# Kernel optimization log

Hardware: AMD Instinct MI355X
Metric: run time of the kernel (lower is better)

## Reference

```python
import jax, jax.numpy as jnp
import numpy as np
import math

NFREQ = 257
NFILTERS = 64
IN_DIM = 64
HIDDEN = 128
SR = 16000
B = 2
T = 1000


def _mel_bounds():
    # Exact replica of FreqCompression.__init__ bound computation (htk mel scale).
    all_freqs = np.linspace(0.0, SR // 2, NFREQ)
    m_max = 2595.0 * math.log10(1.0 + (SR / 2.0) / 700.0)
    m_pts = np.linspace(0.0, m_max, NFILTERS + 2)
    f_pts = 700.0 * (10.0 ** (m_pts / 2595.0) - 1.0)
    bounds = [0]
    for i in range(1, NFILTERS + 1):
        bounds.append(int(np.argmax(all_freqs > f_pts[i])))
    bounds.append(NFREQ)
    return bounds


def setup_inputs() -> dict:
    key = jax.random.key(0)
    k1, k2 = jax.random.split(key)
    bounds = _mel_bounds()
    widths = np.array([bounds[f + 2] - bounds[f] for f in range(NFILTERS)])
    jmax = int(widths.max())
    starts = np.array(bounds[:NFILTERS])
    # per-band freq-bin gather indices, clamped padding
    idx = np.clip(starts[:, None] + np.arange(jmax)[None, :], 0, NFREQ - 1)
    mask = (np.arange(jmax)[None, :] < widths[:, None]).astype(np.float32)  # (F, Jmax)
    x = jax.random.normal(k1, (B, IN_DIM, T, NFREQ), dtype=jnp.float32)
    # Padded ragged trans1 weights: band f uses a (HIDDEN, width_f*IN_DIM) Linear (no bias).
    # Zero-masked beyond each band's true width so padded gather lanes contribute nothing.
    W = jax.random.normal(k2, (NFILTERS, HIDDEN, IN_DIM, jmax), dtype=jnp.float32) * 0.05
    W = W * jnp.asarray(mask)[:, None, None, :]
    return {"x": x, "W": W, "idx": jnp.asarray(idx, jnp.int32), "inverse": 0}


def reference(x, W, idx, inverse):
    # Forward (compression) branch of FreqCompression.forward (inverse == 0).
    # Original: x -> (B, T, in_dim, F); per band f: flatten x[..., bounds[f]:bounds[f+2]]
    # over (in_dim, width) and apply bias-free Linear -> (B, T, hidden); stack over bands
    # and permute to (B, hidden, T, nfilters). Expressed as one padded gather + einsum:
    # x: (B, C, T, F_full); idx: (F, J); W: (F, H, C, J) zero-masked past band width.
    xg = x[:, :, :, idx]  # (B, C, T, F, J)
    out = jnp.einsum('bctfj,fhcj->bhtf', xg, W)  # (B, H, T, F)
    return out
```

## Files before the change

kernel.cpp:

```cpp
#include <hip/hip_runtime.h>
#include <hip/hip_bf16.h>

#define B_    2
#define C_    64
#define T_    1000
#define NF_   257
#define F_    64
#define H_    128
#define NFP_  288

typedef __bf16  bfv8  __attribute__((ext_vector_type(8)));
typedef float   f32x4 __attribute__((ext_vector_type(4)));
typedef short   s16x8 __attribute__((ext_vector_type(8)));

#define GLOBAL_AS __attribute__((address_space(1)))
#define SHARED_AS __attribute__((address_space(3)))

static __device__ __forceinline__ short f2bf(float f) {
  __hip_bfloat16 h = __float2bfloat16(f);
  return *reinterpret_cast<short*>(&h);
}
static __device__ __forceinline__ float bf2f(short s) {
  __hip_bfloat16 h = *reinterpret_cast<__hip_bfloat16*>(&s);
  return __bfloat162float(h);
}

static __device__ __forceinline__ void gload_lds16(const void* g, void* l) {
  __builtin_amdgcn_global_load_lds((const GLOBAL_AS void*)g, (SHARED_AS void*)l, 16, 0, 0);
}

__global__ __launch_bounds__(256) void xprep_kernel(const float* __restrict__ x,
                                                    short* __restrict__ xT) {
  __shared__ float Ls[64][33];
  const int k0 = blockIdx.x * 32;
  const int t  = blockIdx.y;
  const int b  = blockIdx.z;
  {
    const int k  = threadIdx.x & 31;
    const int cb = threadIdx.x >> 5;
#pragma unroll
    for (int i = 0; i < 8; ++i) {
      int c = cb + 8 * i;
      float f = 0.0f;
      int kk = k0 + k;
      if (kk < NF_) f = x[(((size_t)(b * C_ + c)) * T_ + t) * NF_ + kk];
      Ls[c][k] = f;
    }
  }
  __syncthreads();
  {
    const int k  = threadIdx.x >> 3;
    const int c0 = (threadIdx.x & 7) * 8;
    s16x8 v;
#pragma unroll
    for (int i = 0; i < 8; ++i) v[i] = f2bf(Ls[c0 + i][k]);
    *reinterpret_cast<s16x8*>(&xT[(((size_t)(b * T_ + t)) * NFP_ + k0 + k) * C_ + c0]) = v;
  }
}

__global__ __launch_bounds__(256) void wprep_kernel(const float* __restrict__ W,
                                                    short* __restrict__ Wp,
                                                    int* __restrict__ wwidth,
                                                    int jmax, int JPAD) {
  extern __shared__ short Lw[];
  __shared__ int smax;
  const int f  = blockIdx.x >> 4;
  const int h8 = (blockIdx.x & 15) * 8;
  const int tid = threadIdx.x;
  if (tid == 0) smax = 0;
  __syncthreads();
  const int chunk = 8 * C_ * jmax;
  const float* src = W + ((size_t)(f * H_ + h8)) * C_ * jmax;
  int lm = -1;
  for (int o = tid; o < chunk; o += 256) {
    float v = src[o];
    Lw[o] = f2bf(v);
    if (v != 0.0f) { int j = o % jmax; if (j > lm) lm = j; }
  }
  atomicMax(&smax, lm + 1);
  __syncthreads();
  if (tid == 0) atomicMax(&wwidth[f], smax);
  const int KP = C_ * JPAD;
  const int nv = 8 * JPAD * 8;
  for (int id = tid; id < nv; id += 256) {
    int c0 = (id & 7) * 8;
    int j  = (id >> 3) % JPAD;
    int h  = (id >> 3) / JPAD;
    s16x8 v;
    if (j < jmax) {
#pragma unroll
      for (int u = 0; u < 8; ++u) v[u] = Lw[h * C_ * jmax + (c0 + u) * jmax + j];
    } else {
      short z = f2bf(0.0f);
#pragma unroll
      for (int u = 0; u < 8; ++u) v[u] = z;
    }
    *reinterpret_cast<s16x8*>(&Wp[((size_t)(f * H_ + h8 + h)) * KP + j * C_ + c0]) = v;
  }
}

__global__ __launch_bounds__(256) void gemm_kernel(const short* __restrict__ xT,
                                                   const short* __restrict__ Wp,
                                                   const int* __restrict__ idx,
                                                   const int* __restrict__ wwidth,
                                                   short* __restrict__ tmp,
                                                   int jmax, int JPAD) {
  __shared__ short As[2][128 * 64];
  __shared__ short Ws[2][128 * 64];
  const int id = blockIdx.x;
  const int sw = (id & 7) * 128 + (id >> 3);
  const int f  = sw & 63;
  const int tb = sw >> 6;
  const int tt = tb & 7;
  const int b  = tb >> 3;
  const int t0 = tt * 128;
  const int tid  = threadIdx.x;
  const int wave = tid >> 6;
  const int lane = tid & 63;
  const int wm = wave >> 1, wn = wave & 1;
  const int start = idx[f * jmax];
  const int KP = C_ * JPAD;
  int wf = wwidth[f];
  if (wf > JPAD) wf = JPAD;

  const int lrow = lane >> 3;
  const int lsw  = ((lane & 7) ^ lrow) * 8;
  const int l7   = lane & 7;

  f32x4 acc[4][4] = {};

#define STAGE(J, BSEL)                                                              \
  {                                                                                 \
    _Pragma("unroll")                                                               \
    for (int i = 0; i < 4; ++i) {                                                   \
      int tc = t0 + wave * 32 + i * 8 + lrow; if (tc >= T_) tc = T_ - 1;            \
      gload_lds16(&xT[(((size_t)(b * T_ + tc)) * NFP_ + (start + (J))) * C_ + lsw], \
                  &As[BSEL][(wave * 32 + i * 8) * 64]);                             \
    }                                                                               \
    _Pragma("unroll")                                                               \
    for (int i = 0; i < 4; ++i) {                                                   \
      int h = wave * 32 + i * 8 + lrow;                                             \
      gload_lds16(&Wp[((size_t)(f * H_ + h)) * KP + (J) * 64 + lsw],                \
                  &Ws[BSEL][(wave * 32 + i * 8) * 64]);                             \
    }                                                                               \
  }

  if (wf > 0) STAGE(0, 0);
  if (wf > 1) STAGE(1, 1);
  asm volatile("" ::: "memory");
  __builtin_amdgcn_sched_barrier(0);

  for (int j = 0; j < wf; ++j) {
    const int cur = j & 1;
    if (j + 1 < wf) asm volatile("s_waitcnt vmcnt(8)" ::: "memory");
    else            asm volatile("s_waitcnt vmcnt(0)" ::: "memory");
    __builtin_amdgcn_sched_barrier(0);
    asm volatile("s_barrier" ::: "memory");
    __builtin_amdgcn_sched_barrier(0);

#pragma unroll
    for (int ks = 0; ks < 2; ++ks) {
      bfv8 a[4], w[4];
#pragma unroll
      for (int mi = 0; mi < 4; ++mi) {
        int rA = wm * 64 + mi * 16 + (lane & 15);
        int sA = ((ks * 4 + (lane >> 4)) ^ l7) * 8;
        a[mi] = *reinterpret_cast<const bfv8*>(&As[cur][rA * 64 + sA]);
      }
#pragma unroll
      for (int ni = 0; ni < 4; ++ni) {
        int rB = wn * 64 + ni * 16 + (lane & 15);
        int sB = ((ks * 4 + (lane >> 4)) ^ l7) * 8;
        w[ni] = *reinterpret_cast<const bfv8*>(&Ws[cur][rB * 64 + sB]);
      }
#pragma unroll
      for (int mi = 0; mi < 4; ++mi)
#pragma unroll
        for (int ni = 0; ni < 4; ++ni)
          acc[mi][ni] = __builtin_amdgcn_mfma_f32_16x16x32_bf16(a[mi], w[ni], acc[mi][ni], 0, 0, 0);
    }

    __builtin_amdgcn_sched_barrier(0);
    asm volatile("s_barrier" ::: "memory");
    __builtin_amdgcn_sched_barrier(0);
    if (j + 2 < wf) STAGE(j + 2, cur);
    asm volatile("" ::: "memory");
  }
#undef STAGE

  short* obase = tmp + ((size_t)(b * F_ + f)) * T_ * H_;
#pragma unroll
  for (int mi = 0; mi < 4; ++mi) {
#pragma unroll
    for (int q = 0; q < 4; ++q) {
      int t = t0 + wm * 64 + mi * 16 + (lane >> 4) * 4 + q;
      if (t < T_) {
#pragma unroll
        for (int ni = 0; ni < 4; ++ni) {
          int h = wn * 64 + ni * 16 + (lane & 15);
          obase[(size_t)t * H_ + h] = f2bf(acc[mi][ni][q]);
        }
      }
    }
  }
}

__global__ __launch_bounds__(256) void trans_kernel(const short* __restrict__ tmp,
                                                    float* __restrict__ out) {
  __shared__ float L[64][129];
  const int t = blockIdx.x;
  const int b = blockIdx.y;
  {
    const int h0 = (threadIdx.x & 15) * 8;
    const int fb = threadIdx.x >> 4;
#pragma unroll
    for (int i = 0; i < 4; ++i) {
      int f = fb + 16 * i;
      s16x8 v = *reinterpret_cast<const s16x8*>(
          &tmp[(((size_t)(b * F_ + f)) * T_ + t) * H_ + h0]);
#pragma unroll
      for (int u = 0; u < 8; ++u) L[f][h0 + u] = bf2f(v[u]);
    }
  }
  __syncthreads();
  {
    const int fo = threadIdx.x & 63;
    const int h0 = threadIdx.x >> 6;
#pragma unroll
    for (int i = 0; i < 32; ++i) {
      int h = h0 * 32 + i;
      out[(((size_t)(b * H_ + h)) * T_ + t) * F_ + fo] = L[fo][h];
    }
  }
}

__global__ __launch_bounds__(256) void naive_kernel(const float* __restrict__ x,
                                                    const float* __restrict__ W,
                                                    const int* __restrict__ idx,
                                                    float* __restrict__ out,
                                                    int jmax, size_t n) {
  size_t o = (size_t)blockIdx.x * 256 + threadIdx.x;
  if (o >= n) return;
  int f = (int)(o & 63);
  size_t r = o >> 6;
  int t = (int)(r % T_); r /= T_;
  int h = (int)(r % H_);
  int b = (int)(r / H_);
  float s = 0.0f;
  for (int c = 0; c < C_; ++c) {
    const float* xr = x + (((size_t)(b * C_ + c)) * T_ + t) * NF_;
    const float* wr = W + (((size_t)(f * H_ + h)) * C_ + c) * jmax;
    for (int j = 0; j < jmax; ++j) s += xr[idx[f * jmax + j]] * wr[j];
  }
  out[o] = s;
}

extern "C" void kernel_launch(void* const* d_in, const int* in_sizes, int n_in,
                              void* d_out, int out_size, void* d_ws, size_t ws_size,
                              hipStream_t stream) {
  const float* x  = (const float*)d_in[0];
  const float* W  = (const float*)d_in[1];
  const int* idx  = (const int*)d_in[2];
  float* out      = (float*)d_out;

  const int jmax = in_sizes[2] / F_;
  const int JPAD = (jmax + 7) & ~7;

  const size_t xbytes = (size_t)B_ * T_ * NFP_ * C_ * 2;
  const size_t wbytes = (size_t)F_ * H_ * C_ * JPAD * 2;
  const size_t tbytes = (size_t)B_ * F_ * T_ * H_ * 2;
  const size_t wwbytes = 256;
  const size_t lws = (size_t)8 * C_ * jmax * 2;

  if (JPAD <= 32 && ws_size >= xbytes + wbytes + tbytes + wwbytes && lws <= 48 * 1024) {
    short* xT   = (short*)d_ws;
    short* Wp   = (short*)((char*)d_ws + xbytes);
    short* tmp  = (short*)((char*)d_ws + xbytes + wbytes);
    int* wwidth = (int*)((char*)d_ws + xbytes + wbytes + tbytes);

    hipLaunchKernelGGL(xprep_kernel, dim3(NFP_ / 32, T_, B_), dim3(256), 0, stream, x, xT);
    hipLaunchKernelGGL(wprep_kernel, dim3(F_ * 16), dim3(256), lws, stream,
                       W, Wp, wwidth, jmax, JPAD);
    hipLaunchKernelGGL(gemm_kernel, dim3(1024), dim3(256), 0, stream,
                       xT, Wp, idx, wwidth, tmp, jmax, JPAD);
    hipLaunchKernelGGL(trans_kernel, dim3(T_, B_), dim3(256), 0, stream, tmp, out);
  } else {
    const size_t n = (size_t)B_ * H_ * T_ * F_;
    hipLaunchKernelGGL(naive_kernel, dim3((unsigned)((n + 255) / 256)), dim3(256), 0, stream,
                       x, W, idx, out, jmax, n);
  }
}
```

Baseline: 339.5 us.

## Restructure x transpose kernel to process full rows with vectorized loads

The x preparation kernel now handles one (b,t) pair per block, with each wave loading entire 257-element rows using aligned float4 loads and converting to bf16 in shared memory. A rotated read order avoids bank conflicts when writing the transposed [k][c] layout. Before, each block did a 32-wide strided slice with scalar loads. The GEMM inner MFMA loop also gains s_setprio hints to favour math waves. Fewer, larger blocks may reduce occupancy in the prep kernel.

```diff
diff --git a/kernel.cpp b/kernel.cpp
--- a/kernel.cpp
+++ b/kernel.cpp
@@ -31,30 +31,48 @@
 
 __global__ __launch_bounds__(256) void xprep_kernel(const float* __restrict__ x,
                                                     short* __restrict__ xT) {
-  __shared__ float Ls[64][33];
-  const int k0 = blockIdx.x * 32;
-  const int t  = blockIdx.y;
-  const int b  = blockIdx.z;
-  {
-    const int k  = threadIdx.x & 31;
-    const int cb = threadIdx.x >> 5;
-#pragma unroll
-    for (int i = 0; i < 8; ++i) {
-      int c = cb + 8 * i;
-      float f = 0.0f;
-      int kk = k0 + k;
-      if (kk < NF_) f = x[(((size_t)(b * C_ + c)) * T_ + t) * NF_ + kk];
-      Ls[c][k] = f;
-    }
+  __shared__ short Ls[64][268];
+  const int t = blockIdx.x;
+  const int b = blockIdx.y;
+  const int wave = threadIdx.x >> 6;
+  const int lane = threadIdx.x & 63;
+#pragma unroll
+  for (int r = 0; r < 16; ++r) {
+    const int c = wave * 16 + r;
+    const size_t off = (((size_t)(b * C_ + c)) * T_ + t) * NF_;
+    const float* row = x + off;
+    const int pre = (int)((4 - (off & 3)) & 3);
+    const int nv  = (NF_ - pre) >> 2;
+    const int rem = NF_ - pre - 4 * nv;
+    if (lane < pre) Ls[c][lane] = f2bf(row[lane]);
+    if (lane < nv) {
+      f32x4 v4 = *reinterpret_cast<const f32x4*>(row + pre + 4 * lane);
+#pragma unroll
+      for (int u = 0; u < 4; ++u) Ls[c][pre + 4 * lane + u] = f2bf(v4[u]);
+    }
+    if (lane < rem) Ls[c][pre + 4 * nv + lane] = f2bf(row[pre + 4 * nv + lane]);
   }
   __syncthreads();
   {
-    const int k  = threadIdx.x >> 3;
-    const int c0 = (threadIdx.x & 7) * 8;
-    s16x8 v;
-#pragma unroll
-    for (int i = 0; i < 8; ++i) v[i] = f2bf(Ls[c0 + i][k]);
-    *reinterpret_cast<s16x8*>(&xT[(((size_t)(b * T_ + t)) * NFP_ + k0 + k) * C_ + c0]) = v;
+    const int q  = threadIdx.x & 7;
+    const int c0 = q * 8;
+    short* obase = &xT[((size_t)(b * T_ + t)) * NFP_ * C_];
+#pragma unroll
+    for (int it = 0; it < 9; ++it) {
+      int k = it * 32 + (threadIdx.x >> 3);
+      s16x8 v;
+      if (k < NF_) {
+#pragma unroll
+        for (int u = 0; u < 8; ++u) {
+          int ue = (u + q) & 7;
+          v[ue] = Ls[c0 + ue][k];
+        }
+      } else {
+#pragma unroll
+        for (int u = 0; u < 8; ++u) v[u] = 0;
+      }
+      *reinterpret_cast<s16x8*>(&obase[(size_t)k * C_ + c0]) = v;
+    }
   }
 }
 
@@ -91,7 +109,7 @@
 #pragma unroll
       for (int u = 0; u < 8; ++u) v[u] = Lw[h * C_ * jmax + (c0 + u) * jmax + j];
     } else {
-      short z = f2bf(0.0f);
+      short z = 0;
 #pragma unroll
       for (int u = 0; u < 8; ++u) v[u] = z;
     }
@@ -173,11 +191,13 @@
         int sB = ((ks * 4 + (lane >> 4)) ^ l7) * 8;
         w[ni] = *reinterpret_cast<const bfv8*>(&Ws[cur][rB * 64 + sB]);
       }
+      __builtin_amdgcn_s_setprio(1);
 #pragma unroll
       for (int mi = 0; mi < 4; ++mi)
 #pragma unroll
         for (int ni = 0; ni < 4; ++ni)
           acc[mi][ni] = __builtin_amdgcn_mfma_f32_16x16x32_bf16(a[mi], w[ni], acc[mi][ni], 0, 0, 0);
+      __builtin_amdgcn_s_setprio(0);
     }
 
     __builtin_amdgcn_sched_barrier(0);
@@ -278,7 +298,7 @@
     short* tmp  = (short*)((char*)d_ws + xbytes + wbytes);
     int* wwidth = (int*)((char*)d_ws + xbytes + wbytes + tbytes);
 
-    hipLaunchKernelGGL(xprep_kernel, dim3(NFP_ / 32, T_, B_), dim3(256), 0, stream, x, xT);
+    hipLaunchKernelGGL(xprep_kernel, dim3(T_, B_), dim3(256), 0, stream, x, xT);
     hipLaunchKernelGGL(wprep_kernel, dim3(F_ * 16), dim3(256), lws, stream,
                        W, Wp, wwidth, jmax, JPAD);
     hipLaunchKernelGGL(gemm_kernel, dim3(1024), dim3(256), 0, stream,
```

Measured after the change: 351.8 us. 3.6% more time.
